# Performance work log

Hardware: AMD Instinct MI355X
Metric: run time of the kernel (lower is better)

The kernel has to match this reference:

```python
import jax, jax.numpy as jnp
import numpy as np

FPS_RATIO = 0.1
K = 20
EPS = 1e-6
COS_EPS = 1e-8  # torch nn.CosineSimilarity default eps


def setup_inputs() -> dict:
    key = jax.random.key(0)
    k1, k2 = jax.random.split(key)
    N = 40000
    pos = jax.random.normal(k1, (N, 3), dtype=jnp.float32) * 10.0   # spatial coordinates
    vec_pred = jax.random.normal(k2, (N, 3), dtype=jnp.float32)     # predicted direction vectors
    return {"vec_pred": vec_pred, "pos": pos}


def _fps(pos, n_anchors):
    """Deterministic farthest point sampling starting from point 0. Returns [n_anchors] int32."""
    d0 = jnp.sum((pos - pos[0]) ** 2, axis=-1)  # [N]
    def body(min_d, _):
        idx = jnp.argmax(min_d)
        d = jnp.sum((pos - pos[idx]) ** 2, axis=-1)
        return jnp.minimum(min_d, d), idx.astype(jnp.int32)
    _, idxs = jax.lax.scan(body, d0, None, length=n_anchors - 1)
    return jnp.concatenate([jnp.zeros((1,), jnp.int32), idxs])


def _vec_loss(vec_pred, pos):
    N = pos.shape[0]
    n_anchors = int(np.ceil(FPS_RATIO * N))
    anchors = _fps(pos, n_anchors)
    anchors_pos = pos[anchors]                                     # [A, 3]
    # Brute-force KNN: squared distances anchors -> all points, [A, N]
    d2 = (jnp.sum(anchors_pos ** 2, -1, keepdims=True)
          - 2.0 * anchors_pos @ pos.T
          + jnp.sum(pos ** 2, -1)[None, :])
    _, nn_idx = jax.lax.top_k(-d2, K)                              # [A, K]
    nbhds = pos[nn_idx]                                            # [A, K, 3]
    # pca_lowrank: center then SVD; principal direction = top right singular vector
    centered = nbhds - jnp.mean(nbhds, axis=1, keepdims=True)
    _, _, vh = jnp.linalg.svd(centered, full_matrices=False)       # vh: [A, 3, 3]
    vecs = vh[:, 0, :]                                             # [A, 3]
    # Faithful to original: index[0] (anchor ids, each repeated K times) indexes BOTH tensors
    idx0 = jnp.repeat(jnp.arange(n_anchors), K)                    # [A*K]
    a = vec_pred[idx0]
    b = vecs[idx0]
    denom = (jnp.maximum(jnp.linalg.norm(a, axis=-1), COS_EPS)
             * jnp.maximum(jnp.linalg.norm(b, axis=-1), COS_EPS))
    abs_cos = jnp.abs(jnp.sum(a * b, axis=-1) / denom)
    return -jnp.mean(jnp.log(abs_cos + EPS))


def reference(vec_pred, pos):
    # single graph -> forward's average over graphs is just this scalar
    return _vec_loss(vec_pred, pos)
```

## Files before the change

### kernel.cpp

```cpp
#include <hip/hip_runtime.h>
#include <math.h>

#define N_PTS       40000
#define N_ANCH      4000
#define KNN         20
#define NFB         128
#define BT          64
#define NWAVES      128
#define STRIDE      (NWAVES * 64)
#define PPT         5
#define TW          4
#define POOL        (NWAVES * TW)
#define RSLOTS      (POOL / 64)
#define CCAP        6

typedef unsigned long long ull;

#define LD_RLX(p)    __hip_atomic_load((p),  __ATOMIC_RELAXED, __HIP_MEMORY_SCOPE_AGENT)
#define ST_REL(p,v)  __hip_atomic_store((p), (v), __ATOMIC_RELEASE, __HIP_MEMORY_SCOPE_AGENT)
#define ST_RLX(p,v)  __hip_atomic_store((p), (v), __ATOMIC_RELAXED, __HIP_MEMORY_SCOPE_AGENT)


__device__ __forceinline__ double dist64(double px, double py, double pz,
                                         double wx, double wy, double wz) {
  double dx = px - wx, dy = py - wy, dz = pz - wz;
  return dx * dx + dy * dy + dz * dz;
}

__device__ __forceinline__ unsigned key32(double v) {
  unsigned hi = (unsigned)__double2hiint(v);
  return (hi & 0x80000000u) ? ~hi : (hi | 0x80000000u);
}

__device__ __forceinline__ unsigned wave_umax_dpp(unsigned x) {
#define DPP_STEP(ctrl) { unsigned y = (unsigned)__builtin_amdgcn_update_dpp( \
      0, (int)x, ctrl, 0xf, 0xf, true); x = (y > x) ? y : x; }
  DPP_STEP(0x111)
  DPP_STEP(0x112)
  DPP_STEP(0x114)
  DPP_STEP(0x118)
  DPP_STEP(0x142)
  DPP_STEP(0x143)
#undef DPP_STEP
  return (unsigned)__builtin_amdgcn_readlane((int)x, 63);
}

__device__ __forceinline__ int rl_i(int v, int l) { return __builtin_amdgcn_readlane(v, l); }
__device__ __forceinline__ double rl_d(double v, int l) {
  int lo = __builtin_amdgcn_readlane(__double2loint(v), l);
  int hi = __builtin_amdgcn_readlane(__double2hiint(v), l);
  return __hiloint2double(hi, lo);
}

__device__ __forceinline__ void wave_argmax_exact(double& wv, int& wix) {
#pragma unroll
  for (int off = 1; off < 64; off <<= 1) {
    double ov = __shfl_xor(wv, off);
    int    oi = __shfl_xor(wix, off);
    bool bt = (ov > wv) || (ov == wv && oi < wix);
    wv = bt ? ov : wv; wix = bt ? oi : wix;
  }
}

__device__ __forceinline__ void wave_pick(double v, int idx,
                                          unsigned& wkey, int& wlane, int& widx) {
  unsigned k = key32(v);
  unsigned M = wave_umax_dpp(k);
  ull mask = __ballot(k == M);
  if (__popcll(mask) == 1) {
    wlane = __ffsll(mask) - 1;
    widx  = rl_i(idx, wlane);
    wkey  = M;
  } else {
    double wv = v; int wi = idx;
    wave_argmax_exact(wv, wi);
    widx = wi;
    wkey = key32(wv);
    ull m2 = __ballot(idx == widx);
    wlane = __ffsll(m2) - 1;
  }
}

struct FpsSm {
  double lv[CCAP * 64];
  float  lc[CCAP * 64][3];
  int    li[CCAP * 64];
};
struct KnnSm { int w[KNN]; };
union Smem { FpsSm f; KnnSm k; };

__device__ static inline void eig3_maxvec(double xx, double xy, double xz,
                                          double yy, double yz, double zz,
                                          double& v0, double& v1, double& v2) {
  double q  = (xx + yy + zz) / 3.0;
  double p1 = xy * xy + xz * xz + yz * yz;
  double a00 = xx - q, a11 = yy - q, a22 = zz - q;
  double p2 = a00 * a00 + a11 * a11 + a22 * a22 + 2.0 * p1;
  if (p2 < 1e-300) { v0 = 1.0; v1 = 0.0; v2 = 0.0; return; }
  double p   = sqrt(p2 / 6.0);
  double inv = 1.0 / p;
  double b00 = a00 * inv, b01 = xy * inv, b02 = xz * inv;
  double b11 = a11 * inv, b12 = yz * inv, b22 = a22 * inv;
  double detB = b00 * (b11 * b22 - b12 * b12)
              - b01 * (b01 * b22 - b12 * b02)
              + b02 * (b01 * b12 - b11 * b02);
  double r = fmin(1.0, fmax(-1.0, detB * 0.5));
  double phi = acos(r) / 3.0;
  double lam = q + 2.0 * p * cos(phi);

  double r0x = xx - lam, r0y = xy,       r0z = xz;
  double r1x = xy,       r1y = yy - lam, r1z = yz;
  double r2x = xz,       r2y = yz,       r2z = zz - lam;
  double c0x = r0y * r1z - r0z * r1y, c0y = r0z * r1x - r0x * r1z, c0z = r0x * r1y - r0y * r1x;
  double c1x = r0y * r2z - r0z * r2y, c1y = r0z * r2x - r0x * r2z, c1z = r0x * r2y - r0y * r2x;
  double c2x = r1y * r2z - r1z * r2y, c2y = r1z * r2x - r1x * r2z, c2z = r1x * r2y - r1y * r2x;
  double n0 = c0x * c0x + c0y * c0y + c0z * c0z;
  double n1 = c1x * c1x + c1y * c1y + c1z * c1z;
  double n2 = c2x * c2x + c2y * c2y + c2z * c2z;
  double bx = c0x, by = c0y, bz = c0z, bn = n0;
  if (n1 > bn) { bx = c1x; by = c1y; bz = c1z; bn = n1; }
  if (n2 > bn) { bx = c2x; by = c2y; bz = c2z; bn = n2; }
  if (bn < 1e-280) { v0 = 1.0; v1 = 0.0; v2 = 0.0; return; }
  double s = 1.0 / sqrt(bn);
  v0 = bx * s; v1 = by * s; v2 = bz * s;
}

__global__ __launch_bounds__(BT, 2) void fps_knn_kernel(
    const float* __restrict__ pos, const float* __restrict__ vec_pred,
    int* __restrict__ flag, ull* __restrict__ slots,
    int* __restrict__ anchors, double* __restrict__ acc) {
  __shared__ Smem sm;
  const int lane = threadIdx.x & 63;

  if (blockIdx.x < NFB) {
    const int gw   = blockIdx.x;
    const int gtid = gw * 64 + lane;

    double pdx[PPT], pdy[PPT], pdz[PPT], md[PPT];
    const double a0x = (double)pos[0], a0y = (double)pos[1], a0z = (double)pos[2];
#pragma unroll
    for (int k = 0; k < PPT; ++k) {
      int i = gtid + k * STRIDE;
      if (i < N_PTS) {
        pdx[k] = (double)pos[3 * i];
        pdy[k] = (double)pos[3 * i + 1];
        pdz[k] = (double)pos[3 * i + 2];
        md[k]  = dist64(pdx[k], pdy[k], pdz[k], a0x, a0y, a0z);
      } else {
        pdx[k] = 0.0; pdy[k] = 0.0; pdz[k] = 0.0;
        md[k]  = -1.0e300;
      }
    }
    if (gw == 0 && lane == 0) ST_RLX(anchors + 0, 0);

    double bv = -1.0e301; int bi = 0x7fffffff;
#pragma unroll
    for (int k = 0; k < PPT; ++k) {
      int i = gtid + k * STRIDE;
      bool bt = (md[k] > bv) || (md[k] == bv && i < bi);
      bv = bt ? md[k] : bv; bi = bt ? i : bi;
    }

    int nsel  = 1;
    int batch = 0;
#pragma unroll 1
    while (nsel < N_ANCH) {
      batch++;
      const int par = batch & 1;

      unsigned cons = 0;
      double pv = -1.0e301; int pix = 0;
#pragma unroll 1
      for (int r = 0; r < TW; ++r) {
        unsigned wkey; int wlane, widx;
        wave_pick(bv, bi, wkey, wlane, widx);
        double wval = rl_d(bv, wlane);
        if (lane == wlane && bi != 0x7fffffff) {
          cons |= 1u << ((unsigned)(bi - gtid) >> 13);
          bv = -1.0e301; bi = 0x7fffffff;
#pragma unroll
          for (int k = 0; k < PPT; ++k) {
            if (!((cons >> k) & 1u)) {
              int i = gtid + k * STRIDE;
              bool bt = (md[k] > bv) || (md[k] == bv && i < bi);
              bv = bt ? md[k] : bv; bi = bt ? i : bi;
            }
          }
        }
        if (lane == r) { pv = wval; pix = widx; }
      }

      if (lane < TW) {
        ull* sp = slots + (ull)((par * POOL + gw * TW + lane) * 2);
        ST_RLX(sp,     (ull)__double_as_longlong(pv));
        ST_RLX(sp + 1, (ull)(unsigned)pix);
      }
      if (lane == 0) ST_REL(flag + gw, batch);

      for (;;) {
        int f0 = LD_RLX(flag + lane);
        int f1 = LD_RLX(flag + 64 + lane);
        if (__ballot((f0 >= batch) && (f1 >= batch)) == ~0ull) break;
        __builtin_amdgcn_s_sleep(1);
      }
      __builtin_amdgcn_sched_barrier(0);

      double cv[RSLOTS]; int ci[RSLOTS];
#pragma unroll
      for (int j = 0; j < RSLOTS; ++j) {
        ull* sp = slots + (ull)((par * POOL + lane + 64 * j) * 2);
        cv[j] = __longlong_as_double((long long)LD_RLX(sp));
        ci[j] = (int)(unsigned)LD_RLX(sp + 1);
      }

      unsigned kj[RSLOTS];
      unsigned lkmax = 0;
#pragma unroll
      for (int j = 0; j < RSLOTS; ++j) {
        kj[j] = key32(cv[j]);
        lkmax = (kj[j] > lkmax) ? kj[j] : lkmax;
      }
      const unsigned Mkey    = wave_umax_dpp(lkmax);
      const unsigned BmaxKey = wave_umax_dpp(((lane & 3) == 3) ? lkmax : 0u);

      int cap = N_ANCH - nsel;
      int S = 0;

      if (Mkey > BmaxKey) {
        int base = 0;
#pragma unroll
        for (int j = 0; j < RSLOTS; ++j) {
          bool live = kj[j] > BmaxKey;
          ull bal = __ballot(live);
          int rank = base + (int)__popcll(bal & ((1ull << lane) - 1ull));
          if (live) {
            sm.f.lv[rank] = cv[j];
            sm.f.li[rank] = ci[j];
            int p = ci[j];
            sm.f.lc[rank][0] = pos[3 * p];
            sm.f.lc[rank][1] = pos[3 * p + 1];
            sm.f.lc[rank][2] = pos[3 * p + 2];
          }
          base += (int)__popcll(bal);
        }
        const int live_n = base;

        double cv2[CCAP], c2x[CCAP], c2y[CCAP], c2z[CCAP]; int ci2[CCAP];
#pragma unroll
        for (int tt = 0; tt < CCAP; ++tt) {
          if (live_n > tt * 64) {
            int e = tt * 64 + lane;
            bool ok = e < live_n;
            double v  = sm.f.lv[e];
            int    ii = sm.f.li[e];
            float  x  = sm.f.lc[e][0];
            float  y  = sm.f.lc[e][1];
            float  z  = sm.f.lc[e][2];
            cv2[tt] = ok ? v : -1.0e301;
            ci2[tt] = ok ? ii : 0x7fffffff;
            c2x[tt] = ok ? (double)x : 0.0;
            c2y[tt] = ok ? (double)y : 0.0;
            c2z[tt] = ok ? (double)z : 0.0;
          } else {
            cv2[tt] = -1.0e301; ci2[tt] = 0x7fffffff;
            c2x[tt] = 0.0; c2y[tt] = 0.0; c2z[tt] = 0.0;
          }
        }

#pragma unroll 1
        while (S < cap) {
          double wv = cv2[0]; int wix = ci2[0];
          double fx = c2x[0], fy = c2y[0], fz = c2z[0];
#pragma unroll
          for (int tt = 1; tt < CCAP; ++tt) {
            if (live_n > tt * 64) {
              bool bt = (cv2[tt] > wv) || (cv2[tt] == wv && ci2[tt] < wix);
              wv = bt ? cv2[tt] : wv; wix = bt ? ci2[tt] : wix;
              fx = bt ? c2x[tt] : fx; fy = bt ? c2y[tt] : fy; fz = bt ? c2z[tt] : fz;
            }
          }
          unsigned wkey; int wlane, widx;
          wave_pick(wv, wix, wkey, wlane, widx);
          if (S != 0 && !(wkey > BmaxKey)) break;
          double wxd = rl_d(fx, wlane), wyd = rl_d(fy, wlane), wzd = rl_d(fz, wlane);
          if (gw == 0 && lane == 0) ST_RLX(anchors + nsel + S, widx);
#pragma unroll
          for (int tt = 0; tt < CCAP; ++tt) {
            if (live_n > tt * 64) {
              cv2[tt] = fmin(cv2[tt], dist64(c2x[tt], c2y[tt], c2z[tt], wxd, wyd, wzd));
              if (ci2[tt] == widx) cv2[tt] = -1.0e301;
            }
          }
#pragma unroll
          for (int k = 0; k < PPT; ++k)
            md[k] = fmin(md[k], dist64(pdx[k], pdy[k], pdz[k], wxd, wyd, wzd));
          S++;
        }
      } else {
#pragma unroll 1
        while (S < cap) {
          double wv = cv[0]; int wix = ci[0];
#pragma unroll
          for (int j = 1; j < RSLOTS; ++j) {
            bool bt = (cv[j] > wv) || (cv[j] == wv && ci[j] < wix);
            wv = bt ? cv[j] : wv; wix = bt ? ci[j] : wix;
          }
          unsigned wkey; int wlane, widx;
          wave_pick(wv, wix, wkey, wlane, widx);
          if (S != 0 && !(wkey > BmaxKey)) break;
          double wxd = (double)pos[3 * widx];
          double wyd = (double)pos[3 * widx + 1];
          double wzd = (double)pos[3 * widx + 2];
          if (gw == 0 && lane == 0) ST_RLX(anchors + nsel + S, widx);
#pragma unroll
          for (int j = 0; j < RSLOTS; ++j) {
            int p = ci[j];
            double d = dist64((double)pos[3 * p], (double)pos[3 * p + 1],
                              (double)pos[3 * p + 2], wxd, wyd, wzd);
            cv[j] = fmin(cv[j], d);
            if (ci[j] == widx) cv[j] = -1.0e301;
          }
#pragma unroll
          for (int k = 0; k < PPT; ++k)
            md[k] = fmin(md[k], dist64(pdx[k], pdy[k], pdz[k], wxd, wyd, wzd));
          S++;
        }
      }
      nsel += S;

      bv = -1.0e301; bi = 0x7fffffff;
#pragma unroll
      for (int k = 0; k < PPT; ++k) {
        int i = gtid + k * STRIDE;
        bool bt = (md[k] > bv) || (md[k] == bv && i < bi);
        bv = bt ? md[k] : bv; bi = bt ? i : bi;
      }
    }
  } else {
    const int aidx = blockIdx.x - NFB;
    int a = -1;
    for (;;) {
      if (lane == 0) a = LD_RLX(anchors + aidx);
      a = __shfl(a, 0);
      if (a >= 0) break;
      __builtin_amdgcn_s_sleep(32);
    }
    const int ai = a;
    const float ax = pos[3 * ai], ay = pos[3 * ai + 1], az = pos[3 * ai + 2];

    ull key[KNN];
#pragma unroll
    for (int s = 0; s < KNN; ++s) key[s] = ~0ull;
    ull kmax = ~0ull; int smax = 0;
#pragma unroll 1
    for (int k = 0; k < N_PTS / 64; ++k) {
      int j = (k << 6) + lane;
      float dx = pos[3 * j] - ax, dy = pos[3 * j + 1] - ay, dz = pos[3 * j + 2] - az;
      float d  = dx * dx + dy * dy + dz * dz;
      ull nk = ((ull)__float_as_uint(d) << 32) | (unsigned)j;
      if (nk < kmax) {
#pragma unroll
        for (int s = 0; s < KNN; ++s) key[s] = (s == smax) ? nk : key[s];
        kmax = 0ull; smax = 0;
#pragma unroll
        for (int s = 0; s < KNN; ++s) {
          bool g = key[s] > kmax;
          kmax = g ? key[s] : kmax;
          smax = g ? s : smax;
        }
      }
    }

    ull lmin = ~0ull; int ls = 0;
#pragma unroll
    for (int s = 0; s < KNN; ++s) {
      bool l = key[s] < lmin;
      lmin = l ? key[s] : lmin; ls = l ? s : ls;
    }
#pragma unroll 1
    for (int r = 0; r < KNN; ++r) {
      ull g = lmin;
#pragma unroll
      for (int off = 1; off < 64; off <<= 1) {
        ull ov = __shfl_xor(g, off);
        g = (ov < g) ? ov : g;
      }
      if (lane == 0) sm.k.w[r] = (int)(g & 0xffffffffull);
      if (lmin == g) {
#pragma unroll
        for (int s = 0; s < KNN; ++s) key[s] = (s == ls) ? ~0ull : key[s];
        lmin = ~0ull; ls = 0;
#pragma unroll
        for (int s = 0; s < KNN; ++s) {
          bool l = key[s] < lmin;
          lmin = l ? key[s] : lmin; ls = l ? s : ls;
        }
      }
    }

    if (lane == 0) {
      double mx = 0, my = 0, mz = 0;
      for (int r = 0; r < KNN; ++r) {
        int p = sm.k.w[r];
        mx += (double)pos[3 * p]; my += (double)pos[3 * p + 1]; mz += (double)pos[3 * p + 2];
      }
      mx /= KNN; my /= KNN; mz /= KNN;
      double xx = 0, xy = 0, xz = 0, yy = 0, yz = 0, zz = 0;
      for (int r = 0; r < KNN; ++r) {
        int p = sm.k.w[r];
        double cx = (double)pos[3 * p]     - mx;
        double cy = (double)pos[3 * p + 1] - my;
        double cz = (double)pos[3 * p + 2] - mz;
        xx += cx * cx; xy += cx * cy; xz += cx * cz;
        yy += cy * cy; yz += cy * cz; zz += cz * cz;
      }
      double v0, v1, v2;
      eig3_maxvec(xx, xy, xz, yy, yz, zz, v0, v1, v2);

      double a0 = vec_pred[3 * aidx], a1 = vec_pred[3 * aidx + 1], a2 = vec_pred[3 * aidx + 2];
      double an = sqrt(a0 * a0 + a1 * a1 + a2 * a2);
      double bn = sqrt(v0 * v0 + v1 * v1 + v2 * v2);
      double denom = fmax(an, 1e-8) * fmax(bn, 1e-8);
      double c = fabs((a0 * v0 + a1 * v1 + a2 * v2) / denom);
      atomicAdd(acc, log(c + 1e-6));
    }
  }
}

__global__ void finalize_kernel(const double* __restrict__ acc, float* __restrict__ out) {
  out[0] = (float)(-acc[0] / (double)N_ANCH);
}

extern "C" void kernel_launch(void* const* d_in, const int* in_sizes, int n_in,
                              void* d_out, int out_size, void* d_ws, size_t ws_size,
                              hipStream_t stream) {
  (void)in_sizes; (void)n_in; (void)out_size; (void)ws_size;
  const float* vec_pred = (const float*)d_in[0];
  const float* pos      = (const float*)d_in[1];
  float* out = (float*)d_out;

  char* ws = (char*)d_ws;
  double* acc     = (double*)(ws + 0);
  int*    flag    = (int*)(ws + 64);
  ull*    slots   = (ull*)(ws + 1024);
  int*    anchors = (int*)(ws + 17408);

  hipMemsetAsync(ws, 0, 1024, stream);
  hipMemsetAsync(ws + 17408, 0xFF, N_ANCH * 4, stream);
  hipLaunchKernelGGL(fps_knn_kernel, dim3(NFB + N_ANCH), dim3(BT), 0, stream,
                     pos, vec_pred, flag, slots, anchors, acc);
  hipLaunchKernelGGL(finalize_kernel, dim3(1), dim3(1), 0, stream, acc, out);
}
```

Before: 3.206 ms.

## Add two-tier candidate pool for FPS batch selection with deferred distance replay

Doubles the per-wave candidate pool (TW 4→8) and splits the batched FPS selection into two tiers. A small top tier (above the second-best key per group of 8) is consumed first with cheap 2-slot registers. The lower tier is built only if needed, and replays the saved winner coordinates to update its distances. The goal is to pick more anchors per global synchronization round while keeping the common inner loop cheap. The cost is extra shared memory, register pressure from the 8-slot arrays, and more complex control flow.

```diff
diff --git a/kernel.cpp b/kernel.cpp
--- a/kernel.cpp
+++ b/kernel.cpp
@@ -9,10 +9,12 @@
 #define NWAVES      128
 #define STRIDE      (NWAVES * 64)
 #define PPT         5
-#define TW          4
+#define TW          8
 #define POOL        (NWAVES * TW)
 #define RSLOTS      (POOL / 64)
-#define CCAP        6
+#define ACAP        2
+#define BCAP        8
+#define WCAP        128
 
 typedef unsigned long long ull;
 
@@ -82,9 +84,10 @@
 }
 
 struct FpsSm {
-  double lv[CCAP * 64];
-  float  lc[CCAP * 64][3];
-  int    li[CCAP * 64];
+  double lv[BCAP * 64];
+  float  lc[BCAP * 64][3];
+  int    li[BCAP * 64];
+  double wcs[WCAP][3];
 };
 struct KnnSm { int w[KNN]; };
 union Smem { FpsSm f; KnnSm k; };
@@ -221,80 +224,177 @@
         lkmax = (kj[j] > lkmax) ? kj[j] : lkmax;
       }
       const unsigned Mkey    = wave_umax_dpp(lkmax);
-      const unsigned BmaxKey = wave_umax_dpp(((lane & 3) == 3) ? lkmax : 0u);
+      const unsigned T1Key   = wave_umax_dpp(((lane & 7) == 1) ? lkmax : 0u);
+      const unsigned BmaxKey = wave_umax_dpp(((lane & 7) == 7) ? lkmax : 0u);
+
+      int live_n = 0;
+#pragma unroll
+      for (int j = 0; j < RSLOTS; ++j)
+        live_n += (int)__popcll(__ballot(kj[j] > BmaxKey));
 
       int cap = N_ANCH - nsel;
       int S = 0;
-
-      if (Mkey > BmaxKey) {
-        int base = 0;
-#pragma unroll
-        for (int j = 0; j < RSLOTS; ++j) {
-          bool live = kj[j] > BmaxKey;
-          ull bal = __ballot(live);
-          int rank = base + (int)__popcll(bal & ((1ull << lane) - 1ull));
-          if (live) {
-            sm.f.lv[rank] = cv[j];
-            sm.f.li[rank] = ci[j];
-            int p = ci[j];
-            sm.f.lc[rank][0] = pos[3 * p];
-            sm.f.lc[rank][1] = pos[3 * p + 1];
-            sm.f.lc[rank][2] = pos[3 * p + 2];
-          }
-          base += (int)__popcll(bal);
-        }
-        const int live_n = base;
-
-        double cv2[CCAP], c2x[CCAP], c2y[CCAP], c2z[CCAP]; int ci2[CCAP];
-#pragma unroll
-        for (int tt = 0; tt < CCAP; ++tt) {
-          if (live_n > tt * 64) {
-            int e = tt * 64 + lane;
-            bool ok = e < live_n;
-            double v  = sm.f.lv[e];
-            int    ii = sm.f.li[e];
-            float  x  = sm.f.lc[e][0];
-            float  y  = sm.f.lc[e][1];
-            float  z  = sm.f.lc[e][2];
-            cv2[tt] = ok ? v : -1.0e301;
-            ci2[tt] = ok ? ii : 0x7fffffff;
-            c2x[tt] = ok ? (double)x : 0.0;
-            c2y[tt] = ok ? (double)y : 0.0;
-            c2z[tt] = ok ? (double)z : 0.0;
-          } else {
-            cv2[tt] = -1.0e301; ci2[tt] = 0x7fffffff;
-            c2x[tt] = 0.0; c2y[tt] = 0.0; c2z[tt] = 0.0;
-          }
-        }
-
-#pragma unroll 1
-        while (S < cap) {
-          double wv = cv2[0]; int wix = ci2[0];
-          double fx = c2x[0], fy = c2y[0], fz = c2z[0];
-#pragma unroll
-          for (int tt = 1; tt < CCAP; ++tt) {
-            if (live_n > tt * 64) {
-              bool bt = (cv2[tt] > wv) || (cv2[tt] == wv && ci2[tt] < wix);
-              wv = bt ? cv2[tt] : wv; wix = bt ? ci2[tt] : wix;
-              fx = bt ? c2x[tt] : fx; fy = bt ? c2y[tt] : fy; fz = bt ? c2z[tt] : fz;
-            }
-          }
-          unsigned wkey; int wlane, widx;
-          wave_pick(wv, wix, wkey, wlane, widx);
-          if (S != 0 && !(wkey > BmaxKey)) break;
-          double wxd = rl_d(fx, wlane), wyd = rl_d(fy, wlane), wzd = rl_d(fz, wlane);
-          if (gw == 0 && lane == 0) ST_RLX(anchors + nsel + S, widx);
-#pragma unroll
-          for (int tt = 0; tt < CCAP; ++tt) {
-            if (live_n > tt * 64) {
-              cv2[tt] = fmin(cv2[tt], dist64(c2x[tt], c2y[tt], c2z[tt], wxd, wyd, wzd));
-              if (ci2[tt] == widx) cv2[tt] = -1.0e301;
-            }
-          }
-#pragma unroll
-          for (int k = 0; k < PPT; ++k)
-            md[k] = fmin(md[k], dist64(pdx[k], pdy[k], pdz[k], wxd, wyd, wzd));
-          S++;
+      const ull lt = (1ull << lane) - 1ull;
+
+      if (Mkey > BmaxKey && live_n <= BCAP * 64) {
+        int n1 = 0;
+        {
+          int base = 0;
+#pragma unroll
+          for (int j = 0; j < RSLOTS; ++j) {
+            bool t1 = kj[j] > T1Key;
+            ull bal = __ballot(t1);
+            int rank = base + (int)__popcll(bal & lt);
+            if (t1) {
+              sm.f.lv[rank] = cv[j];
+              sm.f.li[rank] = ci[j];
+              int p = ci[j];
+              sm.f.lc[rank][0] = pos[3 * p];
+              sm.f.lc[rank][1] = pos[3 * p + 1];
+              sm.f.lc[rank][2] = pos[3 * p + 2];
+            }
+            base += (int)__popcll(bal);
+          }
+          n1 = base;
+        }
+        double av[ACAP], axr[ACAP], ayr[ACAP], azr[ACAP]; int air[ACAP];
+#pragma unroll
+        for (int tt = 0; tt < ACAP; ++tt) {
+          int e = tt * 64 + lane;
+          bool ok = e < n1;
+          av[tt]  = ok ? sm.f.lv[e] : -1.0e301;
+          air[tt] = ok ? sm.f.li[e] : 0x7fffffff;
+          axr[tt] = ok ? (double)sm.f.lc[e][0] : 0.0;
+          ayr[tt] = ok ? (double)sm.f.lc[e][1] : 0.0;
+          azr[tt] = ok ? (double)sm.f.lc[e][2] : 0.0;
+        }
+
+        if (n1 > 0) {
+#pragma unroll 1
+          while (S < cap) {
+            double wv = av[0]; int wix = air[0];
+            double fx = axr[0], fy = ayr[0], fz = azr[0];
+            if (n1 > 64) {
+              bool bt = (av[1] > wv) || (av[1] == wv && air[1] < wix);
+              wv = bt ? av[1] : wv; wix = bt ? air[1] : wix;
+              fx = bt ? axr[1] : fx; fy = bt ? ayr[1] : fy; fz = bt ? azr[1] : fz;
+            }
+            unsigned wkey; int wlane, widx;
+            wave_pick(wv, wix, wkey, wlane, widx);
+            if (S != 0 && !(wkey > T1Key)) break;
+            double wxd = rl_d(fx, wlane), wyd = rl_d(fy, wlane), wzd = rl_d(fz, wlane);
+            if (lane == 0 && S < WCAP) {
+              sm.f.wcs[S][0] = wxd; sm.f.wcs[S][1] = wyd; sm.f.wcs[S][2] = wzd;
+            }
+            if (gw == 0 && lane == 0) ST_RLX(anchors + nsel + S, widx);
+#pragma unroll
+            for (int tt = 0; tt < ACAP; ++tt) {
+              if (n1 > tt * 64) {
+                av[tt] = fmin(av[tt], dist64(axr[tt], ayr[tt], azr[tt], wxd, wyd, wzd));
+                if (air[tt] == widx) av[tt] = -1.0e301;
+              }
+            }
+#pragma unroll
+            for (int k = 0; k < PPT; ++k)
+              md[k] = fmin(md[k], dist64(pdx[k], pdy[k], pdz[k], wxd, wyd, wzd));
+            S++;
+          }
+        }
+        const int S1 = S;
+
+        if (S < cap) {
+          int base = 0;
+#pragma unroll
+          for (int tt = 0; tt < ACAP; ++tt) {
+            bool keep = (n1 > tt * 64) && (key32(av[tt]) > BmaxKey);
+            ull bal = __ballot(keep);
+            int rank = base + (int)__popcll(bal & lt);
+            if (keep) {
+              sm.f.lv[rank] = av[tt];
+              sm.f.li[rank] = air[tt];
+              sm.f.lc[rank][0] = (float)axr[tt];
+              sm.f.lc[rank][1] = (float)ayr[tt];
+              sm.f.lc[rank][2] = (float)azr[tt];
+            }
+            base += (int)__popcll(bal);
+          }
+          const int n_fresh = base;
+#pragma unroll
+          for (int j = 0; j < RSLOTS; ++j) {
+            bool t2 = (kj[j] > BmaxKey) && !(kj[j] > T1Key);
+            ull bal = __ballot(t2);
+            int rank = base + (int)__popcll(bal & lt);
+            if (t2) {
+              int p = ci[j];
+              sm.f.lv[rank] = cv[j];
+              sm.f.li[rank] = p;
+              sm.f.lc[rank][0] = pos[3 * p];
+              sm.f.lc[rank][1] = pos[3 * p + 1];
+              sm.f.lc[rank][2] = pos[3 * p + 2];
+            }
+            base += (int)__popcll(bal);
+          }
+          const int n2 = base;
+
+          double bvv[BCAP], bxr[BCAP], byr[BCAP], bzr[BCAP]; int bir[BCAP];
+#pragma unroll
+          for (int tt = 0; tt < BCAP; ++tt) {
+            if (n2 > tt * 64) {
+              int e = tt * 64 + lane;
+              bool ok = e < n2;
+              bvv[tt] = ok ? sm.f.lv[e] : -1.0e301;
+              bir[tt] = ok ? sm.f.li[e] : 0x7fffffff;
+              bxr[tt] = ok ? (double)sm.f.lc[e][0] : 0.0;
+              byr[tt] = ok ? (double)sm.f.lc[e][1] : 0.0;
+              bzr[tt] = ok ? (double)sm.f.lc[e][2] : 0.0;
+            } else {
+              bvv[tt] = -1.0e301; bir[tt] = 0x7fffffff;
+              bxr[tt] = 0.0; byr[tt] = 0.0; bzr[tt] = 0.0;
+            }
+          }
+
+#pragma unroll 1
+          for (int s = 0; s < S1; ++s) {
+            double wx = sm.f.wcs[s][0], wy = sm.f.wcs[s][1], wz = sm.f.wcs[s][2];
+#pragma unroll
+            for (int tt = 0; tt < BCAP; ++tt) {
+              if (n2 > tt * 64 && (tt * 64 + 63) >= n_fresh) {
+                int e = tt * 64 + lane;
+                if (e >= n_fresh)
+                  bvv[tt] = fmin(bvv[tt], dist64(bxr[tt], byr[tt], bzr[tt], wx, wy, wz));
+              }
+            }
+          }
+
+#pragma unroll 1
+          while (S < cap) {
+            double wv = bvv[0]; int wix = bir[0];
+            double fx = bxr[0], fy = byr[0], fz = bzr[0];
+#pragma unroll
+            for (int tt = 1; tt < BCAP; ++tt) {
+              if (n2 > tt * 64) {
+                bool bt = (bvv[tt] > wv) || (bvv[tt] == wv && bir[tt] < wix);
+                wv = bt ? bvv[tt] : wv; wix = bt ? bir[tt] : wix;
+                fx = bt ? bxr[tt] : fx; fy = bt ? byr[tt] : fy; fz = bt ? bzr[tt] : fz;
+              }
+            }
+            unsigned wkey; int wlane, widx;
+            wave_pick(wv, wix, wkey, wlane, widx);
+            if (S != 0 && !(wkey > BmaxKey)) break;
+            double wxd = rl_d(fx, wlane), wyd = rl_d(fy, wlane), wzd = rl_d(fz, wlane);
+            if (gw == 0 && lane == 0) ST_RLX(anchors + nsel + S, widx);
+#pragma unroll
+            for (int tt = 0; tt < BCAP; ++tt) {
+              if (n2 > tt * 64) {
+                bvv[tt] = fmin(bvv[tt], dist64(bxr[tt], byr[tt], bzr[tt], wxd, wyd, wzd));
+                if (bir[tt] == widx) bvv[tt] = -1.0e301;
+              }
+            }
+#pragma unroll
+            for (int k = 0; k < PPT; ++k)
+              md[k] = fmin(md[k], dist64(pdx[k], pdy[k], pdz[k], wxd, wyd, wzd));
+            S++;
+          }
         }
       } else {
 #pragma unroll 1
@@ -443,10 +543,10 @@
   double* acc     = (double*)(ws + 0);
   int*    flag    = (int*)(ws + 64);
   ull*    slots   = (ull*)(ws + 1024);
-  int*    anchors = (int*)(ws + 17408);
+  int*    anchors = (int*)(ws + 33792);
 
   hipMemsetAsync(ws, 0, 1024, stream);
-  hipMemsetAsync(ws + 17408, 0xFF, N_ANCH * 4, stream);
+  hipMemsetAsync(ws + 33792, 0xFF, N_ANCH * 4, stream);
   hipLaunchKernelGGL(fps_knn_kernel, dim3(NFB + N_ANCH), dim3(BT), 0, stream,
                      pos, vec_pred, flag, slots, anchors, acc);
   hipLaunchKernelGGL(finalize_kernel, dim3(1), dim3(1), 0, stream, acc, out);
```

New measurement: 4.312 ms. 34.5% more time.
